# Optimization experiments

Hardware: AMD Instinct MI355X
Metric: run time of the kernel (lower is better)

## Reference

```python
import jax, jax.numpy as jnp
import numpy as np

TGT, SRC, BATCH, HID, ATT = 64, 64, 32, 512, 512

def setup_inputs() -> dict:
    key = jax.random.key(0)
    k1, k2, k3, k4 = jax.random.split(key, 4)
    h_t = jax.random.normal(k1, (TGT, BATCH, HID), dtype=jnp.float32)
    src_encodings = jax.random.normal(k2, (SRC, BATCH, HID), dtype=jnp.float32)
    # Wa: Linear(2*HID -> ATT, bias=False); stored as (in, out) for jnp.
    Wa = jax.random.normal(k3, (2 * HID, ATT), dtype=jnp.float32) * (1.0 / np.sqrt(2 * HID))
    # Va: Linear(ATT -> 1, bias=False)
    Va = jax.random.normal(k4, (ATT,), dtype=jnp.float32) * (1.0 / np.sqrt(ATT))
    return {"h_t": h_t, "src_encodings": src_encodings, "Wa": Wa, "Va": Va}

def reference(h_t, src_encodings, Wa, Va):
    # Wa([h_t, src]) = h_t @ Wa_h + src @ Wa_s (exact by linearity of concat-matmul)
    Wa_h, Wa_s = Wa[:HID], Wa[HID:]                 # (H, A) each
    h_part = jnp.einsum('tbh,ha->tba', h_t, Wa_h)   # (T, B, A)
    s_part = jnp.einsum('sbh,ha->sba', src_encodings, Wa_s)  # (S, B, A)
    # scores[s, t, b] = Va . tanh(h_part[t,b] + s_part[s,b])
    hidden = jnp.tanh(h_part[None, :, :, :] + s_part[:, None, :, :])  # (S, T, B, A)
    scores = jnp.einsum('stba,a->stb', hidden, Va)  # (S, T, B)
    attn = jax.nn.softmax(scores, axis=0)           # softmax over src dim
    # context[t,b,:] = sum_s attn[s,t,b] * src[s,b,:]
    context = jnp.einsum('stb,sbh->tbh', attn, src_encodings)  # (T, B, H)
    return context
```

## Files before the change

kernel.cpp:

```cpp
#include <hip/hip_runtime.h>
#include <hip/hip_bf16.h>

#define TGT   64
#define SRCN  64
#define BATCH 32
#define HID   512
#define ATT   512
#define MROWS (TGT * BATCH)

typedef __bf16 bf16_t;
typedef __bf16 bf16x8 __attribute__((ext_vector_type(8)));
typedef float  f32x4  __attribute__((ext_vector_type(4)));

__device__ __forceinline__ float fast_exp2(float x) {
#if __has_builtin(__builtin_amdgcn_exp2f)
  return __builtin_amdgcn_exp2f(x);
#else
  float r; asm("v_exp_f32 %0, %1\n\ts_nop 1" : "=v"(r) : "v"(x)); return r;
#endif
}
__device__ __forceinline__ float fast_rcp(float x) {
#if __has_builtin(__builtin_amdgcn_rcpf)
  return __builtin_amdgcn_rcpf(x);
#else
  float r; asm("v_rcp_f32 %0, %1\n\ts_nop 1" : "=v"(r) : "v"(x)); return r;
#endif
}

#define MFMA(a, b, c) __builtin_amdgcn_mfma_f32_16x16x32_bf16((a), (b), (c), 0, 0, 0)

__global__ __launch_bounds__(256) void proj_gemm(
    const float* __restrict__ h_t, const float* __restrict__ srcp,
    const float* __restrict__ Wa, float* __restrict__ C)
{
  const int z = blockIdx.z;
  const float* __restrict__ A = z ? srcp : h_t;
  const int mbase = blockIdx.x * 64;
  const int nbase = blockIdx.y * 64;

  __shared__ bf16_t Ah[64][72];
  __shared__ bf16_t Al[64][72];
  __shared__ bf16_t Bh[64][72];
  __shared__ bf16_t Bl[64][72];

  const int tid  = threadIdx.x;
  const int lane = tid & 63;
  const int wv   = tid >> 6;
  const int wm   = (wv & 1) * 32;
  const int wn   = (wv >> 1) * 32;
  const int l15  = lane & 15;
  const int qd   = lane >> 4;

  const int arow = tid >> 2;
  const int akc  = (tid & 3) * 16;
  const int bn = tid & 63;
  const int bkg = (tid >> 6) * 16;

  const float* Aptr = A + (size_t)(mbase + arow) * HID + akc;
  const float* Bptr = Wa + (size_t)(z * HID + bkg) * ATT + nbase + bn;

  f32x4 acc00 = {0.f, 0.f, 0.f, 0.f};
  f32x4 acc01 = acc00, acc10 = acc00, acc11 = acc00;

  for (int kb = 0; kb < HID; kb += 64) {
    if (kb) __syncthreads();

    {
      float4 a0 = *(const float4*)(Aptr + kb);
      float4 a1 = *(const float4*)(Aptr + kb + 4);
      float4 a2 = *(const float4*)(Aptr + kb + 8);
      float4 a3 = *(const float4*)(Aptr + kb + 12);
      float av[16] = {a0.x, a0.y, a0.z, a0.w, a1.x, a1.y, a1.z, a1.w,
                      a2.x, a2.y, a2.z, a2.w, a3.x, a3.y, a3.z, a3.w};
      bf16x8 hi0, hi1, lo0, lo1;
#pragma unroll
      for (int j = 0; j < 8; ++j) {
        bf16_t h = (bf16_t)av[j];
        hi0[j] = h;
        lo0[j] = (bf16_t)(av[j] - (float)h);
        bf16_t h2 = (bf16_t)av[j + 8];
        hi1[j] = h2;
        lo1[j] = (bf16_t)(av[j + 8] - (float)h2);
      }
      *(bf16x8*)&Ah[arow][akc]     = hi0;
      *(bf16x8*)&Ah[arow][akc + 8] = hi1;
      *(bf16x8*)&Al[arow][akc]     = lo0;
      *(bf16x8*)&Al[arow][akc + 8] = lo1;
    }

    {
      const float* bp = Bptr + (size_t)kb * ATT;
      float bv[16];
#pragma unroll
      for (int j = 0; j < 16; ++j) bv[j] = bp[(size_t)j * ATT];
      bf16x8 hi0, hi1, lo0, lo1;
#pragma unroll
      for (int j = 0; j < 8; ++j) {
        bf16_t h = (bf16_t)bv[j];
        hi0[j] = h;
        lo0[j] = (bf16_t)(bv[j] - (float)h);
        bf16_t h2 = (bf16_t)bv[j + 8];
        hi1[j] = h2;
        lo1[j] = (bf16_t)(bv[j + 8] - (float)h2);
      }
      *(bf16x8*)&Bh[bn][bkg]     = hi0;
      *(bf16x8*)&Bh[bn][bkg + 8] = hi1;
      *(bf16x8*)&Bl[bn][bkg]     = lo0;
      *(bf16x8*)&Bl[bn][bkg + 8] = lo1;
    }
    __syncthreads();

#pragma unroll
    for (int h = 0; h < 2; ++h) {
      const int kh = h * 32 + qd * 8;
      bf16x8 ah0 = *(const bf16x8*)&Ah[wm + l15][kh];
      bf16x8 ah1 = *(const bf16x8*)&Ah[wm + 16 + l15][kh];
      bf16x8 al0 = *(const bf16x8*)&Al[wm + l15][kh];
      bf16x8 al1 = *(const bf16x8*)&Al[wm + 16 + l15][kh];
      bf16x8 bh0 = *(const bf16x8*)&Bh[wn + l15][kh];
      bf16x8 bh1 = *(const bf16x8*)&Bh[wn + 16 + l15][kh];
      bf16x8 bl0 = *(const bf16x8*)&Bl[wn + l15][kh];
      bf16x8 bl1 = *(const bf16x8*)&Bl[wn + 16 + l15][kh];

      acc00 = MFMA(ah0, bh0, acc00);
      acc01 = MFMA(ah0, bh1, acc01);
      acc10 = MFMA(ah1, bh0, acc10);
      acc11 = MFMA(ah1, bh1, acc11);
      acc00 = MFMA(al0, bh0, acc00);
      acc01 = MFMA(al0, bh1, acc01);
      acc10 = MFMA(al1, bh0, acc10);
      acc11 = MFMA(al1, bh1, acc11);
      acc00 = MFMA(ah0, bl0, acc00);
      acc01 = MFMA(ah0, bl1, acc01);
      acc10 = MFMA(ah1, bl0, acc10);
      acc11 = MFMA(ah1, bl1, acc11);
    }
  }

  float* Cz = C + (size_t)z * (MROWS * ATT);
#pragma unroll
  for (int r = 0; r < 4; ++r) {
    int row0 = mbase + wm + qd * 4 + r;
    int row1 = row0 + 16;
    int col0 = nbase + wn + l15;
    Cz[(size_t)row0 * ATT + col0]      = acc00[r];
    Cz[(size_t)row0 * ATT + col0 + 16] = acc01[r];
    Cz[(size_t)row1 * ATT + col0]      = acc10[r];
    Cz[(size_t)row1 * ATT + col0 + 16] = acc11[r];
  }
}

__global__ __launch_bounds__(512) void attn_fused(
    const float* __restrict__ ws, const float* __restrict__ srcp,
    const float* __restrict__ Va, float* __restrict__ out)
{
  const float* __restrict__ h_part = ws;
  const float* __restrict__ s_part = ws + (size_t)TGT * BATCH * ATT;
  const float SC = 2.8853900817779268f;

  const int t0   = blockIdx.x * 4;
  const int b    = blockIdx.y;
  const int tid  = threadIdx.x;
  const int lane = tid & 63;
  const int wv   = tid >> 6;

  __shared__ float scoreLds[4][64];
  __shared__ float attnLds[4][64];

  const int abase = lane * 8;
  float va[8], eH[4][8];
  *(float4*)&va[0] = *(const float4*)(Va + abase);
  *(float4*)&va[4] = *(const float4*)(Va + abase + 4);

  float vsum = 0.f;
#pragma unroll
  for (int j = 0; j < 8; ++j) vsum += va[j];
#pragma unroll
  for (int off = 32; off; off >>= 1) vsum += __shfl_xor(vsum, off);

#pragma unroll
  for (int t = 0; t < 4; ++t) {
    const float* hp = h_part + ((size_t)(t0 + t) * BATCH + b) * ATT + abase;
    float4 h0 = *(const float4*)hp;
    float4 h1 = *(const float4*)(hp + 4);
    float hv[8] = {h0.x, h0.y, h0.z, h0.w, h1.x, h1.y, h1.z, h1.w};
#pragma unroll
    for (int j = 0; j < 8; ++j) eH[t][j] = fast_exp2(hv[j] * SC);
  }

#pragma unroll 2
  for (int i = 0; i < 8; ++i) {
    const int s = wv * 8 + i;
    const float* sp = s_part + ((size_t)s * BATCH + b) * ATT + abase;
    float4 s0 = *(const float4*)sp;
    float4 s1 = *(const float4*)(sp + 4);
    float sv[8] = {s0.x, s0.y, s0.z, s0.w, s1.x, s1.y, s1.z, s1.w};
    float ex[8];
#pragma unroll
    for (int j = 0; j < 8; ++j) ex[j] = fast_exp2(sv[j] * SC);

    float q0 = 0.f, q1 = 0.f, q2 = 0.f, q3 = 0.f;
#pragma unroll
    for (int j = 0; j < 8; ++j) {
      float e = ex[j];
      float vj = va[j];
      float y0 = fmaf(e, eH[0][j], 1.0f);
      float y1 = fmaf(e, eH[1][j], 1.0f);
      float y2 = fmaf(e, eH[2][j], 1.0f);
      float y3 = fmaf(e, eH[3][j], 1.0f);
      float r01 = fast_rcp(y0 * y1);
      float r23 = fast_rcp(y2 * y3);
      q0 = fmaf(vj * y1, r01, q0);
      q1 = fmaf(vj * y0, r01, q1);
      q2 = fmaf(vj * y3, r23, q2);
      q3 = fmaf(vj * y2, r23, q3);
    }
#pragma unroll
    for (int off = 32; off; off >>= 1) {
      q0 += __shfl_xor(q0, off);
      q1 += __shfl_xor(q1, off);
      q2 += __shfl_xor(q2, off);
      q3 += __shfl_xor(q3, off);
    }
    if (lane == 0) {
      scoreLds[0][s] = vsum - 2.0f * q0;
      scoreLds[1][s] = vsum - 2.0f * q1;
      scoreLds[2][s] = vsum - 2.0f * q2;
      scoreLds[3][s] = vsum - 2.0f * q3;
    }
  }
  __syncthreads();

  if (wv < 4) {
    float sc = scoreLds[wv][lane];
    float m = sc;
#pragma unroll
    for (int off = 32; off; off >>= 1) m = fmaxf(m, __shfl_xor(m, off));
    float e = fast_exp2((sc - m) * 1.4426950408889634f);
    float ssum = e;
#pragma unroll
    for (int off = 32; off; off >>= 1) ssum += __shfl_xor(ssum, off);
    attnLds[wv][lane] = e * fast_rcp(ssum);
  }
  __syncthreads();

  {
    float c0 = 0.f, c1 = 0.f, c2 = 0.f, c3 = 0.f;
    const float* sb = srcp + (size_t)b * HID + tid;
#pragma unroll 8
    for (int s = 0; s < SRCN; ++s) {
      float sv = sb[(size_t)s * BATCH * HID];
      c0 = fmaf(attnLds[0][s], sv, c0);
      c1 = fmaf(attnLds[1][s], sv, c1);
      c2 = fmaf(attnLds[2][s], sv, c2);
      c3 = fmaf(attnLds[3][s], sv, c3);
    }
    out[((size_t)(t0 + 0) * BATCH + b) * HID + tid] = c0;
    out[((size_t)(t0 + 1) * BATCH + b) * HID + tid] = c1;
    out[((size_t)(t0 + 2) * BATCH + b) * HID + tid] = c2;
    out[((size_t)(t0 + 3) * BATCH + b) * HID + tid] = c3;
  }
}

extern "C" void kernel_launch(void* const* d_in, const int* in_sizes, int n_in,
                              void* d_out, int out_size, void* d_ws, size_t ws_size,
                              hipStream_t stream) {
  const float* h_t = (const float*)d_in[0];
  const float* src = (const float*)d_in[1];
  const float* Wa  = (const float*)d_in[2];
  const float* Va  = (const float*)d_in[3];
  float* out = (float*)d_out;
  float* C   = (float*)d_ws;

  proj_gemm<<<dim3(32, 8, 2), 256, 0, stream>>>(h_t, src, Wa, C);
  attn_fused<<<dim3(16, 32), 512, 0, stream>>>(C, src, Va, out);
}
```

Baseline: 97.82 us.

## Prefetch s_part rows, hoist GEMM loads, remap attention blocks for L2 locality

In the projection GEMM, the A and B global loads are issued together before either is converted to bf16, so more loads are in flight at once. In the attention kernel, s_part rows are loaded into registers up front and then double-buffered inside a fully unrolled loop, with the Va sum moved after the h_part loads. The grid is flattened and remapped so that consecutive blocks cycle through 8 batches before advancing in t, aiming for better cache reuse of s_part and src. These changes raise register pressure, which may lower occupancy.

```diff
diff --git a/kernel.cpp b/kernel.cpp
--- a/kernel.cpp
+++ b/kernel.cpp
@@ -65,11 +65,16 @@
   for (int kb = 0; kb < HID; kb += 64) {
     if (kb) __syncthreads();
 
+    float4 a0 = *(const float4*)(Aptr + kb);
+    float4 a1 = *(const float4*)(Aptr + kb + 4);
+    float4 a2 = *(const float4*)(Aptr + kb + 8);
+    float4 a3 = *(const float4*)(Aptr + kb + 12);
+    const float* bp = Bptr + (size_t)kb * ATT;
+    float bv[16];
+#pragma unroll
+    for (int j = 0; j < 16; ++j) bv[j] = bp[(size_t)j * ATT];
+
     {
-      float4 a0 = *(const float4*)(Aptr + kb);
-      float4 a1 = *(const float4*)(Aptr + kb + 4);
-      float4 a2 = *(const float4*)(Aptr + kb + 8);
-      float4 a3 = *(const float4*)(Aptr + kb + 12);
       float av[16] = {a0.x, a0.y, a0.z, a0.w, a1.x, a1.y, a1.z, a1.w,
                       a2.x, a2.y, a2.z, a2.w, a3.x, a3.y, a3.z, a3.w};
       bf16x8 hi0, hi1, lo0, lo1;
@@ -89,10 +94,6 @@
     }
 
     {
-      const float* bp = Bptr + (size_t)kb * ATT;
-      float bv[16];
-#pragma unroll
-      for (int j = 0; j < 16; ++j) bv[j] = bp[(size_t)j * ATT];
       bf16x8 hi0, hi1, lo0, lo1;
 #pragma unroll
       for (int j = 0; j < 8; ++j) {
@@ -158,8 +159,10 @@
   const float* __restrict__ s_part = ws + (size_t)TGT * BATCH * ATT;
   const float SC = 2.8853900817779268f;
 
-  const int t0   = blockIdx.x * 4;
-  const int b    = blockIdx.y;
+  const int L  = blockIdx.x;
+  const int b  = (L & 7) + 8 * (L >> 7);
+  const int t0 = ((L >> 3) & 15) * 4;
+
   const int tid  = threadIdx.x;
   const int lane = tid & 63;
   const int wv   = tid >> 6;
@@ -168,16 +171,23 @@
   __shared__ float attnLds[4][64];
 
   const int abase = lane * 8;
+
+  const int s0 = wv * 8;
+  const float* spB = s_part + ((size_t)s0 * BATCH + b) * ATT + abase;
+  float4 P0[4], P1[4];
+#pragma unroll
+  for (int i = 0; i < 4; ++i) {
+    P0[i] = *(const float4*)(spB + (size_t)i * BATCH * ATT);
+    P1[i] = *(const float4*)(spB + (size_t)i * BATCH * ATT + 4);
+  }
+
   float va[8], eH[4][8];
-  *(float4*)&va[0] = *(const float4*)(Va + abase);
-  *(float4*)&va[4] = *(const float4*)(Va + abase + 4);
-
-  float vsum = 0.f;
-#pragma unroll
-  for (int j = 0; j < 8; ++j) vsum += va[j];
-#pragma unroll
-  for (int off = 32; off; off >>= 1) vsum += __shfl_xor(vsum, off);
-
+  {
+    float4 v0 = *(const float4*)(Va + abase);
+    float4 v1 = *(const float4*)(Va + abase + 4);
+    va[0] = v0.x; va[1] = v0.y; va[2] = v0.z; va[3] = v0.w;
+    va[4] = v1.x; va[5] = v1.y; va[6] = v1.z; va[7] = v1.w;
+  }
 #pragma unroll
   for (int t = 0; t < 4; ++t) {
     const float* hp = h_part + ((size_t)(t0 + t) * BATCH + b) * ATT + abase;
@@ -188,13 +198,20 @@
     for (int j = 0; j < 8; ++j) eH[t][j] = fast_exp2(hv[j] * SC);
   }
 
-#pragma unroll 2
+  float vsum = 0.f;
+#pragma unroll
+  for (int j = 0; j < 8; ++j) vsum += va[j];
+#pragma unroll
+  for (int off = 32; off; off >>= 1) vsum += __shfl_xor(vsum, off);
+
+#pragma unroll
   for (int i = 0; i < 8; ++i) {
-    const int s = wv * 8 + i;
-    const float* sp = s_part + ((size_t)s * BATCH + b) * ATT + abase;
-    float4 s0 = *(const float4*)sp;
-    float4 s1 = *(const float4*)(sp + 4);
-    float sv[8] = {s0.x, s0.y, s0.z, s0.w, s1.x, s1.y, s1.z, s1.w};
+    float4 c0 = P0[i & 3], c1 = P1[i & 3];
+    if (i < 4) {
+      P0[i & 3] = *(const float4*)(spB + (size_t)(i + 4) * BATCH * ATT);
+      P1[i & 3] = *(const float4*)(spB + (size_t)(i + 4) * BATCH * ATT + 4);
+    }
+    float sv[8] = {c0.x, c0.y, c0.z, c0.w, c1.x, c1.y, c1.z, c1.w};
     float ex[8];
 #pragma unroll
     for (int j = 0; j < 8; ++j) ex[j] = fast_exp2(sv[j] * SC);
@@ -223,6 +240,7 @@
       q3 += __shfl_xor(q3, off);
     }
     if (lane == 0) {
+      const int s = s0 + i;
       scoreLds[0][s] = vsum - 2.0f * q0;
       scoreLds[1][s] = vsum - 2.0f * q1;
       scoreLds[2][s] = vsum - 2.0f * q2;
@@ -247,7 +265,7 @@
   {
     float c0 = 0.f, c1 = 0.f, c2 = 0.f, c3 = 0.f;
     const float* sb = srcp + (size_t)b * HID + tid;
-#pragma unroll 8
+#pragma unroll 16
     for (int s = 0; s < SRCN; ++s) {
       float sv = sb[(size_t)s * BATCH * HID];
       c0 = fmaf(attnLds[0][s], sv, c0);
@@ -273,5 +291,5 @@
   float* C   = (float*)d_ws;
 
   proj_gemm<<<dim3(32, 8, 2), 256, 0, stream>>>(h_t, src, Wa, C);
-  attn_fused<<<dim3(16, 32), 512, 0, stream>>>(C, src, Va, out);
-}
+  attn_fused<<<512, 512, 0, stream>>>(C, src, Va, out);
+}
```

Result: slower. 102.5 us (+4.8%).

## Widen attention blocks to 8 targets, fold scale into GEMM, reorder workspace by batch

Applied to the files above, without the earlier changes.

Each attention block now handles 8 target positions with 1024 threads, so every exp of an s_part element is reused across twice as many targets. The GEMM epilogue pre-multiplies by the tanh scale and writes rows in batch-major order, so the attention kernel reads contiguous rows and skips the multiply. The GEMM also hoists its A and B global loads ahead of the conversion code, and the attention loop prefetches the next s_part row. The cost is higher register pressure from 64 eH values per thread, and the 1024-thread blocks may reduce occupancy.

```diff
diff --git a/kernel.cpp b/kernel.cpp
--- a/kernel.cpp
+++ b/kernel.cpp
@@ -65,11 +65,16 @@
   for (int kb = 0; kb < HID; kb += 64) {
     if (kb) __syncthreads();
 
+    float4 a0 = *(const float4*)(Aptr + kb);
+    float4 a1 = *(const float4*)(Aptr + kb + 4);
+    float4 a2 = *(const float4*)(Aptr + kb + 8);
+    float4 a3 = *(const float4*)(Aptr + kb + 12);
+    const float* bp = Bptr + (size_t)kb * ATT;
+    float bv[16];
+#pragma unroll
+    for (int j = 0; j < 16; ++j) bv[j] = bp[(size_t)j * ATT];
+
     {
-      float4 a0 = *(const float4*)(Aptr + kb);
-      float4 a1 = *(const float4*)(Aptr + kb + 4);
-      float4 a2 = *(const float4*)(Aptr + kb + 8);
-      float4 a3 = *(const float4*)(Aptr + kb + 12);
       float av[16] = {a0.x, a0.y, a0.z, a0.w, a1.x, a1.y, a1.z, a1.w,
                       a2.x, a2.y, a2.z, a2.w, a3.x, a3.y, a3.z, a3.w};
       bf16x8 hi0, hi1, lo0, lo1;
@@ -87,12 +92,7 @@
       *(bf16x8*)&Al[arow][akc]     = lo0;
       *(bf16x8*)&Al[arow][akc + 8] = lo1;
     }
-
     {
-      const float* bp = Bptr + (size_t)kb * ATT;
-      float bv[16];
-#pragma unroll
-      for (int j = 0; j < 16; ++j) bv[j] = bp[(size_t)j * ATT];
       bf16x8 hi0, hi1, lo0, lo1;
 #pragma unroll
       for (int j = 0; j < 8; ++j) {
@@ -137,38 +137,42 @@
     }
   }
 
+  const float SC = 2.8853900817779268f;
   float* Cz = C + (size_t)z * (MROWS * ATT);
 #pragma unroll
   for (int r = 0; r < 4; ++r) {
-    int row0 = mbase + wm + qd * 4 + r;
-    int row1 = row0 + 16;
+    int m0 = mbase + wm + qd * 4 + r;
+    int m1 = m0 + 16;
+    int row0 = (m0 & 31) * 64 + (m0 >> 5);
+    int row1 = (m1 & 31) * 64 + (m1 >> 5);
     int col0 = nbase + wn + l15;
-    Cz[(size_t)row0 * ATT + col0]      = acc00[r];
-    Cz[(size_t)row0 * ATT + col0 + 16] = acc01[r];
-    Cz[(size_t)row1 * ATT + col0]      = acc10[r];
-    Cz[(size_t)row1 * ATT + col0 + 16] = acc11[r];
-  }
-}
-
-__global__ __launch_bounds__(512) void attn_fused(
+    Cz[(size_t)row0 * ATT + col0]      = acc00[r] * SC;
+    Cz[(size_t)row0 * ATT + col0 + 16] = acc01[r] * SC;
+    Cz[(size_t)row1 * ATT + col0]      = acc10[r] * SC;
+    Cz[(size_t)row1 * ATT + col0 + 16] = acc11[r] * SC;
+  }
+}
+
+__global__ __launch_bounds__(1024, 4) void attn_fused(
     const float* __restrict__ ws, const float* __restrict__ srcp,
     const float* __restrict__ Va, float* __restrict__ out)
 {
   const float* __restrict__ h_part = ws;
   const float* __restrict__ s_part = ws + (size_t)TGT * BATCH * ATT;
-  const float SC = 2.8853900817779268f;
-
-  const int t0   = blockIdx.x * 4;
-  const int b    = blockIdx.y;
+
+  const int bid  = blockIdx.x;
+  const int b    = bid & 31;
+  const int t0   = (bid >> 5) * 8;
   const int tid  = threadIdx.x;
   const int lane = tid & 63;
   const int wv   = tid >> 6;
 
-  __shared__ float scoreLds[4][64];
-  __shared__ float attnLds[4][64];
+  __shared__ float scoreLds[8][64];
+  __shared__ float attnLds[8][64];
 
   const int abase = lane * 8;
-  float va[8], eH[4][8];
+
+  float va[8];
   *(float4*)&va[0] = *(const float4*)(Va + abase);
   *(float4*)&va[4] = *(const float4*)(Va + abase + 4);
 
@@ -178,28 +182,35 @@
 #pragma unroll
   for (int off = 32; off; off >>= 1) vsum += __shfl_xor(vsum, off);
 
-#pragma unroll
-  for (int t = 0; t < 4; ++t) {
-    const float* hp = h_part + ((size_t)(t0 + t) * BATCH + b) * ATT + abase;
+  float eH[8][8];
+#pragma unroll
+  for (int t = 0; t < 8; ++t) {
+    const float* hp = h_part + ((size_t)(b * 64 + t0 + t)) * ATT + abase;
     float4 h0 = *(const float4*)hp;
     float4 h1 = *(const float4*)(hp + 4);
     float hv[8] = {h0.x, h0.y, h0.z, h0.w, h1.x, h1.y, h1.z, h1.w};
 #pragma unroll
-    for (int j = 0; j < 8; ++j) eH[t][j] = fast_exp2(hv[j] * SC);
-  }
-
-#pragma unroll 2
-  for (int i = 0; i < 8; ++i) {
-    const int s = wv * 8 + i;
-    const float* sp = s_part + ((size_t)s * BATCH + b) * ATT + abase;
-    float4 s0 = *(const float4*)sp;
-    float4 s1 = *(const float4*)(sp + 4);
-    float sv[8] = {s0.x, s0.y, s0.z, s0.w, s1.x, s1.y, s1.z, s1.w};
+    for (int j = 0; j < 8; ++j) eH[t][j] = fast_exp2(hv[j]);
+  }
+
+  const int s0 = wv * 4;
+  const float* spB = s_part + ((size_t)(b * 64 + s0)) * ATT + abase;
+  float4 p0 = *(const float4*)spB;
+  float4 p1 = *(const float4*)(spB + 4);
+#pragma unroll
+  for (int i = 0; i < 4; ++i) {
+    float4 c0 = p0, c1 = p1;
+    if (i < 3) {
+      p0 = *(const float4*)(spB + (size_t)(i + 1) * ATT);
+      p1 = *(const float4*)(spB + (size_t)(i + 1) * ATT + 4);
+    }
+    float sv[8] = {c0.x, c0.y, c0.z, c0.w, c1.x, c1.y, c1.z, c1.w};
     float ex[8];
 #pragma unroll
-    for (int j = 0; j < 8; ++j) ex[j] = fast_exp2(sv[j] * SC);
+    for (int j = 0; j < 8; ++j) ex[j] = fast_exp2(sv[j]);
 
     float q0 = 0.f, q1 = 0.f, q2 = 0.f, q3 = 0.f;
+    float q4 = 0.f, q5 = 0.f, q6 = 0.f, q7 = 0.f;
 #pragma unroll
     for (int j = 0; j < 8; ++j) {
       float e = ex[j];
@@ -208,12 +219,22 @@
       float y1 = fmaf(e, eH[1][j], 1.0f);
       float y2 = fmaf(e, eH[2][j], 1.0f);
       float y3 = fmaf(e, eH[3][j], 1.0f);
+      float y4 = fmaf(e, eH[4][j], 1.0f);
+      float y5 = fmaf(e, eH[5][j], 1.0f);
+      float y6 = fmaf(e, eH[6][j], 1.0f);
+      float y7 = fmaf(e, eH[7][j], 1.0f);
       float r01 = fast_rcp(y0 * y1);
       float r23 = fast_rcp(y2 * y3);
+      float r45 = fast_rcp(y4 * y5);
+      float r67 = fast_rcp(y6 * y7);
       q0 = fmaf(vj * y1, r01, q0);
       q1 = fmaf(vj * y0, r01, q1);
       q2 = fmaf(vj * y3, r23, q2);
       q3 = fmaf(vj * y2, r23, q3);
+      q4 = fmaf(vj * y5, r45, q4);
+      q5 = fmaf(vj * y4, r45, q5);
+      q6 = fmaf(vj * y7, r67, q6);
+      q7 = fmaf(vj * y6, r67, q7);
     }
 #pragma unroll
     for (int off = 32; off; off >>= 1) {
@@ -221,17 +242,26 @@
       q1 += __shfl_xor(q1, off);
       q2 += __shfl_xor(q2, off);
       q3 += __shfl_xor(q3, off);
+      q4 += __shfl_xor(q4, off);
+      q5 += __shfl_xor(q5, off);
+      q6 += __shfl_xor(q6, off);
+      q7 += __shfl_xor(q7, off);
     }
     if (lane == 0) {
+      const int s = s0 + i;
       scoreLds[0][s] = vsum - 2.0f * q0;
       scoreLds[1][s] = vsum - 2.0f * q1;
       scoreLds[2][s] = vsum - 2.0f * q2;
       scoreLds[3][s] = vsum - 2.0f * q3;
+      scoreLds[4][s] = vsum - 2.0f * q4;
+      scoreLds[5][s] = vsum - 2.0f * q5;
+      scoreLds[6][s] = vsum - 2.0f * q6;
+      scoreLds[7][s] = vsum - 2.0f * q7;
     }
   }
   __syncthreads();
 
-  if (wv < 4) {
+  if (wv < 8) {
     float sc = scoreLds[wv][lane];
     float m = sc;
 #pragma unroll
@@ -245,20 +275,24 @@
   __syncthreads();
 
   {
+    const int h  = tid & 511;
+    const int tg = tid >> 9;
     float c0 = 0.f, c1 = 0.f, c2 = 0.f, c3 = 0.f;
-    const float* sb = srcp + (size_t)b * HID + tid;
+    const float* sb = srcp + (size_t)b * HID + h;
+    const float* aL = &attnLds[tg * 4][0];
 #pragma unroll 8
     for (int s = 0; s < SRCN; ++s) {
       float sv = sb[(size_t)s * BATCH * HID];
-      c0 = fmaf(attnLds[0][s], sv, c0);
-      c1 = fmaf(attnLds[1][s], sv, c1);
-      c2 = fmaf(attnLds[2][s], sv, c2);
-      c3 = fmaf(attnLds[3][s], sv, c3);
-    }
-    out[((size_t)(t0 + 0) * BATCH + b) * HID + tid] = c0;
-    out[((size_t)(t0 + 1) * BATCH + b) * HID + tid] = c1;
-    out[((size_t)(t0 + 2) * BATCH + b) * HID + tid] = c2;
-    out[((size_t)(t0 + 3) * BATCH + b) * HID + tid] = c3;
+      c0 = fmaf(aL[0 * 64 + s], sv, c0);
+      c1 = fmaf(aL[1 * 64 + s], sv, c1);
+      c2 = fmaf(aL[2 * 64 + s], sv, c2);
+      c3 = fmaf(aL[3 * 64 + s], sv, c3);
+    }
+    const int tb = t0 + tg * 4;
+    out[((size_t)(tb + 0) * BATCH + b) * HID + h] = c0;
+    out[((size_t)(tb + 1) * BATCH + b) * HID + h] = c1;
+    out[((size_t)(tb + 2) * BATCH + b) * HID + h] = c2;
+    out[((size_t)(tb + 3) * BATCH + b) * HID + h] = c3;
   }
 }
 
@@ -273,5 +307,5 @@
   float* C   = (float*)d_ws;
 
   proj_gemm<<<dim3(32, 8, 2), 256, 0, stream>>>(h_t, src, Wa, C);
-  attn_fused<<<dim3(16, 32), 512, 0, stream>>>(C, src, Va, out);
-}
+  attn_fused<<<256, 1024, 0, stream>>>(C, src, Va, out);
+}
```

Result: no change. 98.07 us (+0.2%).
